# Performance work log

Measured on AMD Instinct MI355X. Metric: run time of the kernel, lower is better.

The kernel has to match this reference:

```python
import jax, jax.numpy as jnp
import numpy as np

B, CIN, COUT, K, H, W = 2, 128, 64, 64, 128, 128
BN_EPS = 1e-5


def setup_inputs() -> dict:
    key = jax.random.key(0)
    k1, k2, k3, k4 = jax.random.split(key, 4)
    x = jax.random.normal(k1, (B, CIN, H, W), dtype=jnp.float32)
    index = jax.random.randint(k2, (B, 1, H, W), 0, K)  # superpixel labels
    # kaiming_uniform(a=sqrt(5)) ~ uniform with bound sqrt(6/((1+5)*fan_in)) = 1/sqrt(fan_in)
    Wft = jax.random.uniform(k3, (CIN, COUT), dtype=jnp.float32,
                             minval=-1.0, maxval=1.0) / np.sqrt(CIN).astype(np.float32)
    Wm = jax.random.uniform(k4, (COUT, COUT), dtype=jnp.float32,
                            minval=-1.0, maxval=1.0) / np.sqrt(COUT).astype(np.float32)
    gamma = jnp.ones((COUT,), jnp.float32)
    beta = jnp.zeros((COUT,), jnp.float32)
    return {"x": x, "index": index, "Wft": Wft, "Wm": Wm, "gamma": gamma, "beta": beta}


def _gnn_forward(x, index, Wft, Wm, gamma, beta):
    # FeatureTransform: [B,Cin,H,W] -> [B,Cout,H,W]
    xt = jnp.einsum('bchw,co->bohw', x, Wft)

    idx = index[:, 0]                                   # [B,H,W]
    oh = jax.nn.one_hot(idx, K, dtype=xt.dtype)         # [B,H,W,K]

    # RegionalMeans (segment-mean over superpixels; equivalent to the
    # repeated-tensor multiply+sum in the torch code, without the 5D blowup)
    block_sum = oh.sum(axis=(1, 2))                     # [B,K]
    sums = jnp.einsum('bhwk,bohw->bko', oh, xt)         # [B,K,Cout]
    denom = block_sum + (block_sum == 0).astype(xt.dtype)
    means = sums / denom[..., None]                     # [B,K,Cout]

    # Adj: pairwise Mahalanobis distance with learned cov = Wm @ Wm.T
    cov = Wm @ Wm.T
    inv_cov = jnp.linalg.inv(cov)
    diff = means[:, :, None, :] - means[:, None, :, :]  # [B,K,K,Cout]
    q = jnp.einsum('bijc,cd,bijd->bij', diff, inv_cov, diff)
    dist = jnp.sqrt(jnp.maximum(q, 1e-12))              # clamp: diagonal q==0
    adj = jnp.exp(-dist)                                # [B,K,K]

    # GCN propagate: adjacency-weighted aggregation of region means
    adj_means = jnp.einsum('bij,bjo->bio', adj, means)  # [B,K,Cout]

    # sum_k one_hot_k * (x_rep + adj_means_k) == xt + gather(adj_means, idx)
    gathered = jnp.take_along_axis(adj_means, idx.reshape(B, -1, 1), axis=1)
    gathered = gathered.reshape(B, H, W, COUT).transpose(0, 3, 1, 2)
    features = jax.nn.relu(xt + gathered)               # [B,Cout,H,W]

    # BatchNorm2d (training-mode batch statistics, biased variance)
    mean = features.mean(axis=(0, 2, 3), keepdims=True)
    var = features.var(axis=(0, 2, 3), keepdims=True)
    out = (features - mean) / jnp.sqrt(var + BN_EPS)
    out = out * gamma[None, :, None, None] + beta[None, :, None, None]
    return out


def reference(x, index, Wft, Wm, gamma, beta):
    return _gnn_forward(x, index, Wft, Wm, gamma, beta)
```

## Files before the change

kernel.cpp:

```cpp
#include <hip/hip_runtime.h>
#include <hip/hip_bf16.h>

#define CIN   128
#define COUT  64
#define HW    16384

typedef __hip_bfloat16 bf16;

#define OFF_XT    0u
#define OFF_PS    1048576u
#define OFF_PC    2097152u
#define OFF_MEANS 2129920u
#define OFF_DIAG  2138112u
#define OFF_INV   2138240u
#define OFF_ADJM  2142336u
#define OFF_BNP   2150528u

__device__ __forceinline__ float rdlane(float v, int lane) {
  return __int_as_float(__builtin_amdgcn_readlane(__float_as_int(v), lane));
}
__device__ __forceinline__ unsigned short f2bfu(float f) {
  union { bf16 h; unsigned short u; } cv; cv.h = __float2bfloat16(f); return cv.u;
}
__device__ __forceinline__ float bf2f(unsigned short u) {
  union { unsigned int i; float f; } cv; cv.i = ((unsigned int)u) << 16; return cv.f;
}

__global__ __launch_bounds__(256, 4) void k1_xt_bins_inv(
    const float* __restrict__ x, const int* __restrict__ index,
    const float* __restrict__ Wft, const float* __restrict__ Wm,
    float* __restrict__ ws)
{
  __shared__ __align__(16) float smem[64 * 68];
  const int blk = blockIdx.x, tid = threadIdx.x;
  if (blk < 1024) {
    float* lds_sums = smem;
    float* lds_cnt  = smem + 2304;
    for (int i = tid; i < 2368; i += 256) smem[i] = 0.f;
    __syncthreads();
    const int b  = blk >> 9;
    const int oh = (blk >> 8) & 1;
    const int ps = blk & 255;
    const int w = tid >> 6, lane = tid & 63;
    const int pq = lane & 7, og = lane >> 3;
    const int px = ps * 64 + (w >> 1) * 32 + pq * 4;
    const int lo = (w & 1) * 16 + og * 2;
    const int o  = oh * 32 + lo;
    const float* xp = x + (size_t)b * CIN * HW + px;
    const float* wp = Wft + o;
    const int4 kv = *(const int4*)(index + b * HW + px);
    float acc[8];
#pragma unroll
    for (int j = 0; j < 8; ++j) acc[j] = 0.f;
#pragma unroll 16
    for (int c = 0; c < 128; ++c) {
      const float4 xv = *(const float4*)xp; xp += HW;
      const float2 wv = *(const float2*)wp; wp += 64;
      acc[0] = fmaf(xv.x, wv.x, acc[0]); acc[1] = fmaf(xv.y, wv.x, acc[1]);
      acc[2] = fmaf(xv.z, wv.x, acc[2]); acc[3] = fmaf(xv.w, wv.x, acc[3]);
      acc[4] = fmaf(xv.x, wv.y, acc[4]); acc[5] = fmaf(xv.y, wv.y, acc[5]);
      acc[6] = fmaf(xv.z, wv.y, acc[6]); acc[7] = fmaf(xv.w, wv.y, acc[7]);
    }
    unsigned short* xtu = (unsigned short*)(ws + OFF_XT);
#pragma unroll
    for (int i = 0; i < 2; ++i) {
      ushort4 u;
      u.x = f2bfu(acc[i*4+0]); u.y = f2bfu(acc[i*4+1]);
      u.z = f2bfu(acc[i*4+2]); u.w = f2bfu(acc[i*4+3]);
      *(ushort4*)(xtu + (size_t)(b * 64 + o + i) * HW + px) = u;
    }
    const int kk[4] = {kv.x, kv.y, kv.z, kv.w};
#pragma unroll
    for (int j = 0; j < 4; ++j) {
      atomicAdd(&lds_sums[kk[j] * 36 + lo    ], acc[j]);
      atomicAdd(&lds_sums[kk[j] * 36 + lo + 1], acc[4 + j]);
    }
    if (oh == 0 && (w & 1) == 0 && og == 0) {
#pragma unroll
      for (int j = 0; j < 4; ++j) atomicAdd(&lds_cnt[kk[j]], 1.f);
    }
    __syncthreads();
    unsigned short* pb = (unsigned short*)(ws + OFF_PS) + (size_t)((b * 2 + oh) * 256 + ps) * 2048;
    {
      const int k = tid >> 2, l0 = (tid & 3) * 8;
      const float4 v0 = *(const float4*)&lds_sums[k * 36 + l0];
      const float4 v1 = *(const float4*)&lds_sums[k * 36 + l0 + 4];
      ushort4 ua, ub;
      ua.x = f2bfu(v0.x); ua.y = f2bfu(v0.y); ua.z = f2bfu(v0.z); ua.w = f2bfu(v0.w);
      ub.x = f2bfu(v1.x); ub.y = f2bfu(v1.y); ub.z = f2bfu(v1.z); ub.w = f2bfu(v1.w);
      unsigned short* pp = pb + k * 32 + l0;
      *(ushort4*)pp = ua; *(ushort4*)(pp + 4) = ub;
    }
    if (oh == 0 && tid < 64)
      ws[OFF_PC + (size_t)(b * 64 + tid) * 256 + ps] = lds_cnt[tid];
  } else {
    float* wm = smem;
    for (int e = tid; e < 4096; e += 256) wm[(e >> 6) * 68 + (e & 63)] = Wm[e];
    __syncthreads();
    const int i0 = (tid >> 4) << 2, j0 = (tid & 15) << 2;
    float c4[16];
#pragma unroll
    for (int q = 0; q < 16; ++q) c4[q] = 0.f;
    for (int cq = 0; cq < 64; cq += 4) {
      float4 a[4], bb[4];
#pragma unroll
      for (int ii = 0; ii < 4; ++ii) a[ii]  = *(const float4*)&wm[(i0+ii)*68 + cq];
#pragma unroll
      for (int jj = 0; jj < 4; ++jj) bb[jj] = *(const float4*)&wm[(j0+jj)*68 + cq];
#pragma unroll
      for (int ii = 0; ii < 4; ++ii)
#pragma unroll
        for (int jj = 0; jj < 4; ++jj)
          c4[ii*4+jj] = fmaf(a[ii].x, bb[jj].x, fmaf(a[ii].y, bb[jj].y,
                        fmaf(a[ii].z, bb[jj].z, fmaf(a[ii].w, bb[jj].w, c4[ii*4+jj]))));
    }
    __syncthreads();
#pragma unroll
    for (int ii = 0; ii < 4; ++ii)
#pragma unroll
      for (int jj = 0; jj < 4; ++jj)
        smem[(i0+ii)*68 + (j0+jj)] = c4[ii*4+jj];
    __syncthreads();
    if (tid < 64) {
      __builtin_amdgcn_s_setprio(3);
      float r[64];
#pragma unroll
      for (int j = 0; j < 64; ++j) r[j] = smem[tid * 68 + j];
#pragma unroll
      for (int k = 0; k < 64; ++k) {
        const float piv = rdlane(r[k], k);
        const float rp  = 1.0f / piv;
        const float a   = (tid == k) ? (rp - 1.0f) : (-r[k] * rp);
#pragma unroll
        for (int j = 0; j < 64; ++j) {
          const float s = rdlane(r[j], k);
          r[j] = fmaf(a, s, r[j]);
        }
        r[k] = (tid == k) ? rp : a;
      }
      __builtin_amdgcn_s_setprio(0);
#pragma unroll
      for (int j = 0; j < 64; ++j) ws[OFF_INV + tid * 64 + j] = r[j];
    }
  }
}

__global__ __launch_bounds__(1024) void k15_means_diag(float* __restrict__ ws)
{
  __shared__ float red[1024];
  __shared__ float lds_c[4];
  __shared__ float lds_m[64];
  const int blk = blockIdx.x, t = threadIdx.x;
  const int b = blk >> 6, k = blk & 63;
  const int o = t & 63, chunk = t >> 6;
  const int oh = o >> 5, o32 = o & 31;
  const unsigned short* psu = (const unsigned short*)(ws + OFF_PS);
  const size_t base = (size_t)((b * 2 + oh) * 256 + chunk * 16) * 2048 + k * 32 + o32;
  float s = 0.f;
#pragma unroll
  for (int i = 0; i < 16; ++i) s += bf2f(psu[base + (size_t)i * 2048]);
  red[chunk * 64 + o] = s;
  float cv = 0.f;
  if (t < 256) cv = ws[OFF_PC + (size_t)(b * 64 + k) * 256 + t];
#pragma unroll
  for (int m = 32; m; m >>= 1) cv += __shfl_xor(cv, m, 64);
  if (t < 256 && (t & 63) == 0) lds_c[t >> 6] = cv;
  __syncthreads();
  if (t < 64) {
    float m_raw = 0.f;
#pragma unroll
    for (int ch = 0; ch < 16; ++ch) m_raw += red[ch * 64 + o];
    const float cnt = lds_c[0] + lds_c[1] + lds_c[2] + lds_c[3];
    const float denom = cnt + ((cnt == 0.f) ? 1.f : 0.f);
    const float m = m_raw / denom;
    ws[OFF_MEANS + (size_t)(b * 64 + k) * 64 + o] = m;
    lds_m[o] = m;
    float inner = 0.f;
#pragma unroll 8
    for (int d = 0; d < 64; ++d) inner = fmaf(ws[OFF_INV + d * 64 + o], lds_m[d], inner);
    float p = m * inner;
#pragma unroll
    for (int mm = 32; mm; mm >>= 1) p += __shfl_xor(p, mm, 64);
    if (o == 0) ws[OFF_DIAG + b * 64 + k] = p;
  }
}

__global__ __launch_bounds__(256) void k2_adj(float* __restrict__ ws)
{
  __shared__ __align__(16) float means_s[64 * 68];
  __shared__ __align__(16) float inv_s[64 * 68];
  __shared__ __align__(16) float T_s[8 * 68];
  __shared__ __align__(16) float adj_s[8 * 68];
  __shared__ float diag_s[64];
  const int b = blockIdx.x >> 3;
  const int i0 = (blockIdx.x & 7) << 3;
  const int t = threadIdx.x;
  const float* mg = ws + OFF_MEANS + b * 4096;
  for (int e = t; e < 4096; e += 256) means_s[(e >> 6) * 68 + (e & 63)] = mg[e];
  const float* ig = ws + OFF_INV;
  for (int e = t; e < 4096; e += 256) inv_s[(e >> 6) * 68 + (e & 63)] = ig[e];
  if (t < 64) diag_s[t] = ws[OFF_DIAG + b * 64 + t];
  __syncthreads();
  if (t < 128) {
    const int i = t >> 4, d0 = (t & 15) << 2;
    float4 acc = {0.f, 0.f, 0.f, 0.f};
    for (int c = 0; c < 64; ++c) {
      const float mv = means_s[(i0 + i) * 68 + c];
      const float4 iv = *(const float4*)&inv_s[c * 68 + d0];
      acc.x = fmaf(mv, iv.x, acc.x); acc.y = fmaf(mv, iv.y, acc.y);
      acc.z = fmaf(mv, iv.z, acc.z); acc.w = fmaf(mv, iv.w, acc.w);
    }
    *(float4*)&T_s[i * 68 + d0] = acc;
  }
  __syncthreads();
  {
    const int i = t >> 5, jb = t & 31;
#pragma unroll
    for (int jj = 0; jj < 2; ++jj) {
      const int j = jb + (jj << 5);
      float4 p4 = {0.f, 0.f, 0.f, 0.f};
      for (int dq = 0; dq < 64; dq += 4) {
        const float4 tv = *(const float4*)&T_s[i * 68 + dq];
        const float4 mv = *(const float4*)&means_s[j * 68 + dq];
        p4.x = fmaf(tv.x, mv.x, p4.x); p4.y = fmaf(tv.y, mv.y, p4.y);
        p4.z = fmaf(tv.z, mv.z, p4.z); p4.w = fmaf(tv.w, mv.w, p4.w);
      }
      const float p = (p4.x + p4.y) + (p4.z + p4.w);
      const float q = diag_s[i0 + i] + diag_s[j] - 2.f * p;
      adj_s[i * 68 + j] = __expf(-sqrtf(fmaxf(q, 1e-12f)));
    }
  }
  __syncthreads();
  if (t < 128) {
    const int i = t >> 4, oq = (t & 15) << 2;
    float4 am = {0.f, 0.f, 0.f, 0.f};
    for (int j = 0; j < 64; ++j) {
      const float av = adj_s[i * 68 + j];
      const float4 mv = *(const float4*)&means_s[j * 68 + oq];
      am.x = fmaf(av, mv.x, am.x); am.y = fmaf(av, mv.y, am.y);
      am.z = fmaf(av, mv.z, am.z); am.w = fmaf(av, mv.w, am.w);
    }
    *(float4*)(ws + OFF_ADJM + (size_t)(b * 64 + i0 + i) * 64 + oq) = am;
  }
}

__global__ __launch_bounds__(256) void k3_bnstats(const int* __restrict__ index,
                                                  float* __restrict__ ws)
{
  __shared__ float am_s[128];
  __shared__ float red[4];
  const int blk = blockIdx.x, t = threadIdx.x;
  const int b = blk >> 8, oc = (blk >> 3) & 31, tile = blk & 7;
  const int o0 = oc * 2;
  if (t < 128) am_s[t] = ws[OFF_ADJM + (size_t)(b * 64 + (t >> 1)) * 64 + o0 + (t & 1)];
  if (t < 4) red[t] = 0.f;
  __syncthreads();
  const int lane = t & 63, w = t >> 6;
  const unsigned short* xtu = (const unsigned short*)(ws + OFF_XT);
  float s0 = 0.f, s1 = 0.f, q0 = 0.f, q1 = 0.f;
#pragma unroll
  for (int q = 0; q < 2; ++q) {
    const int px = tile * 2048 + (w * 2 + q) * 256 + lane * 4;
    const int4 kv = *(const int4*)(index + b * HW + px);
    const ushort4 u0 = *(const ushort4*)(xtu + (size_t)(b * 64 + o0    ) * HW + px);
    const ushort4 u1 = *(const ushort4*)(xtu + (size_t)(b * 64 + o0 + 1) * HW + px);
    const int kk[4] = {kv.x, kv.y, kv.z, kv.w};
    const float x0[4] = {bf2f(u0.x), bf2f(u0.y), bf2f(u0.z), bf2f(u0.w)};
    const float x1[4] = {bf2f(u1.x), bf2f(u1.y), bf2f(u1.z), bf2f(u1.w)};
#pragma unroll
    for (int j = 0; j < 4; ++j) {
      const float2 am = *(const float2*)&am_s[kk[j] * 2];
      const float f0 = fmaxf(x0[j] + am.x, 0.f);
      const float f1 = fmaxf(x1[j] + am.y, 0.f);
      s0 += f0; q0 = fmaf(f0, f0, q0);
      s1 += f1; q1 = fmaf(f1, f1, q1);
    }
  }
#pragma unroll
  for (int m = 1; m < 64; m <<= 1) {
    s0 += __shfl_xor(s0, m, 64); s1 += __shfl_xor(s1, m, 64);
    q0 += __shfl_xor(q0, m, 64); q1 += __shfl_xor(q1, m, 64);
  }
  if (lane == 0) {
    atomicAdd(&red[0], s0); atomicAdd(&red[1], s1);
    atomicAdd(&red[2], q0); atomicAdd(&red[3], q1);
  }
  __syncthreads();
  if (t == 0) {
    float4 v; v.x = red[0]; v.y = red[1]; v.z = red[2]; v.w = red[3];
    *(float4*)(ws + OFF_BNP + (size_t)(oc * 16 + b * 8 + tile) * 4) = v;
  }
}

__global__ __launch_bounds__(256) void k4_out(const int* __restrict__ index,
    const float* __restrict__ gamma, const float* __restrict__ beta,
    const float* __restrict__ ws, float* __restrict__ out)
{
  __shared__ float am_s[128];
  __shared__ float4 tmp[16];
  __shared__ float sc_s[2], sh_s[2];
  const int blk = blockIdx.x, t = threadIdx.x;
  const int b = blk >> 8, oc = (blk >> 3) & 31, tile = blk & 7;
  const int o0 = oc * 2;
  if (t < 128) am_s[t] = ws[OFF_ADJM + (size_t)(b * 64 + (t >> 1)) * 64 + o0 + (t & 1)];
  if (t < 16) tmp[t] = *(const float4*)(ws + OFF_BNP + (size_t)(oc * 16 + t) * 4);
  if (t < 2) {
    float s = 0.f, qq = 0.f;
#pragma unroll
    for (int i = 0; i < 16; ++i) {
      const float4 v = tmp[i];
      s  += (t == 0) ? v.x : v.y;
      qq += (t == 0) ? v.z : v.w;
    }
    const float mean = s * (1.f / 32768.f);
    const float var  = qq * (1.f / 32768.f) - mean * mean;
    const float sc = gamma[o0 + t] * rsqrtf(var + 1e-5f);
    sc_s[t] = sc;
    sh_s[t] = fmaf(-mean, sc, beta[o0 + t]);
  }
  __syncthreads();
  const int lane = t & 63, w = t >> 6;
  const unsigned short* xtu = (const unsigned short*)(ws + OFF_XT);
  const float c0 = sc_s[0], c1 = sc_s[1], h0 = sh_s[0], h1 = sh_s[1];
#pragma unroll
  for (int q = 0; q < 2; ++q) {
    const int px = tile * 2048 + (w * 2 + q) * 256 + lane * 4;
    const int4 kv = *(const int4*)(index + b * HW + px);
    const ushort4 u0 = *(const ushort4*)(xtu + (size_t)(b * 64 + o0    ) * HW + px);
    const ushort4 u1 = *(const ushort4*)(xtu + (size_t)(b * 64 + o0 + 1) * HW + px);
    const int kk[4] = {kv.x, kv.y, kv.z, kv.w};
    const float x0[4] = {bf2f(u0.x), bf2f(u0.y), bf2f(u0.z), bf2f(u0.w)};
    const float x1[4] = {bf2f(u1.x), bf2f(u1.y), bf2f(u1.z), bf2f(u1.w)};
    float4 o4a, o4b;
    float* oa = (float*)&o4a; float* ob = (float*)&o4b;
#pragma unroll
    for (int j = 0; j < 4; ++j) {
      const float2 am = *(const float2*)&am_s[kk[j] * 2];
      oa[j] = fmaf(fmaxf(x0[j] + am.x, 0.f), c0, h0);
      ob[j] = fmaf(fmaxf(x1[j] + am.y, 0.f), c1, h1);
    }
    *(float4*)(out + (size_t)(b * 64 + o0    ) * HW + px) = o4a;
    *(float4*)(out + (size_t)(b * 64 + o0 + 1) * HW + px) = o4b;
  }
}

extern "C" void kernel_launch(void* const* d_in, const int* in_sizes, int n_in,
                              void* d_out, int out_size, void* d_ws, size_t ws_size,
                              hipStream_t stream) {
  const float* x     = (const float*)d_in[0];
  const int*   index = (const int*)d_in[1];
  const float* Wft   = (const float*)d_in[2];
  const float* Wm    = (const float*)d_in[3];
  const float* gamma = (const float*)d_in[4];
  const float* beta  = (const float*)d_in[5];
  float* ws  = (float*)d_ws;
  float* out = (float*)d_out;

  k1_xt_bins_inv<<<1025, 256, 0, stream>>>(x, index, Wft, Wm, ws);
  k15_means_diag<<<128, 1024, 0, stream>>>(ws);
  k2_adj<<<16, 256, 0, stream>>>(ws);
  k3_bnstats<<<512, 256, 0, stream>>>(index, ws);
  k4_out<<<512, 256, 0, stream>>>(index, gamma, beta, ws, out);
}
```

Before: 140.6 us.

## Stage x and Wft tiles in LDS and compute all 64 outputs per block

New measurement: 298.0 us. 2.12x slower.

```diff
diff --git a/kernel.cpp b/kernel.cpp
--- a/kernel.cpp
+++ b/kernel.cpp
@@ -26,73 +26,84 @@
   union { unsigned int i; float f; } cv; cv.i = ((unsigned int)u) << 16; return cv.f;
 }
 
-__global__ __launch_bounds__(256, 4) void k1_xt_bins_inv(
+__global__ __launch_bounds__(256, 2) void k1_xt_bins_inv(
     const float* __restrict__ x, const int* __restrict__ index,
     const float* __restrict__ Wft, const float* __restrict__ Wm,
     float* __restrict__ ws)
 {
-  __shared__ __align__(16) float smem[64 * 68];
+  __shared__ __align__(16) float smem[16384];
   const int blk = blockIdx.x, tid = threadIdx.x;
-  if (blk < 1024) {
-    float* lds_sums = smem;
-    float* lds_cnt  = smem + 2304;
-    for (int i = tid; i < 2368; i += 256) smem[i] = 0.f;
-    __syncthreads();
-    const int b  = blk >> 9;
-    const int oh = (blk >> 8) & 1;
-    const int ps = blk & 255;
-    const int w = tid >> 6, lane = tid & 63;
-    const int pq = lane & 7, og = lane >> 3;
-    const int px = ps * 64 + (w >> 1) * 32 + pq * 4;
-    const int lo = (w & 1) * 16 + og * 2;
-    const int o  = oh * 32 + lo;
-    const float* xp = x + (size_t)b * CIN * HW + px;
-    const float* wp = Wft + o;
+  if (blk < 512) {
+    float* xl = smem;
+    float* wl = smem + 8192;
+    const int b = blk >> 8, ps = blk & 255;
+    const float* xg = x + (size_t)b * CIN * HW + ps * 64;
+#pragma unroll
+    for (int j = 0; j < 8; ++j) {
+      const int fj = j * 256 + tid;
+      const int c = fj >> 4, q4 = (fj & 15) * 4;
+      *(float4*)&xl[c * 64 + q4] = *(const float4*)(xg + (size_t)c * HW + q4);
+      *(float4*)&wl[c * 64 + q4] = *(const float4*)(Wft + c * 64 + q4);
+    }
+    __syncthreads();
+    const int px_grp = tid & 15, o_grp = tid >> 4;
+    const int px = ps * 64 + px_grp * 4, o0 = o_grp * 4;
+    float acc[16];
+#pragma unroll
+    for (int j = 0; j < 16; ++j) acc[j] = 0.f;
+#pragma unroll 8
+    for (int c = 0; c < 128; ++c) {
+      const float4 xv = *(const float4*)&xl[c * 64 + px_grp * 4];
+      const float4 wv = *(const float4*)&wl[c * 64 + o0];
+      acc[ 0]=fmaf(xv.x,wv.x,acc[ 0]); acc[ 1]=fmaf(xv.y,wv.x,acc[ 1]);
+      acc[ 2]=fmaf(xv.z,wv.x,acc[ 2]); acc[ 3]=fmaf(xv.w,wv.x,acc[ 3]);
+      acc[ 4]=fmaf(xv.x,wv.y,acc[ 4]); acc[ 5]=fmaf(xv.y,wv.y,acc[ 5]);
+      acc[ 6]=fmaf(xv.z,wv.y,acc[ 6]); acc[ 7]=fmaf(xv.w,wv.y,acc[ 7]);
+      acc[ 8]=fmaf(xv.x,wv.z,acc[ 8]); acc[ 9]=fmaf(xv.y,wv.z,acc[ 9]);
+      acc[10]=fmaf(xv.z,wv.z,acc[10]); acc[11]=fmaf(xv.w,wv.z,acc[11]);
+      acc[12]=fmaf(xv.x,wv.w,acc[12]); acc[13]=fmaf(xv.y,wv.w,acc[13]);
+      acc[14]=fmaf(xv.z,wv.w,acc[14]); acc[15]=fmaf(xv.w,wv.w,acc[15]);
+    }
+    unsigned short* xtu = (unsigned short*)(ws + OFF_XT);
+#pragma unroll
+    for (int oj = 0; oj < 4; ++oj) {
+      ushort4 u;
+      u.x = f2bfu(acc[oj*4+0]); u.y = f2bfu(acc[oj*4+1]);
+      u.z = f2bfu(acc[oj*4+2]); u.w = f2bfu(acc[oj*4+3]);
+      *(ushort4*)(xtu + (size_t)(b * 64 + o0 + oj) * HW + px) = u;
+    }
     const int4 kv = *(const int4*)(index + b * HW + px);
-    float acc[8];
-#pragma unroll
-    for (int j = 0; j < 8; ++j) acc[j] = 0.f;
-#pragma unroll 16
-    for (int c = 0; c < 128; ++c) {
-      const float4 xv = *(const float4*)xp; xp += HW;
-      const float2 wv = *(const float2*)wp; wp += 64;
-      acc[0] = fmaf(xv.x, wv.x, acc[0]); acc[1] = fmaf(xv.y, wv.x, acc[1]);
-      acc[2] = fmaf(xv.z, wv.x, acc[2]); acc[3] = fmaf(xv.w, wv.x, acc[3]);
-      acc[4] = fmaf(xv.x, wv.y, acc[4]); acc[5] = fmaf(xv.y, wv.y, acc[5]);
-      acc[6] = fmaf(xv.z, wv.y, acc[6]); acc[7] = fmaf(xv.w, wv.y, acc[7]);
-    }
-    unsigned short* xtu = (unsigned short*)(ws + OFF_XT);
-#pragma unroll
-    for (int i = 0; i < 2; ++i) {
-      ushort4 u;
-      u.x = f2bfu(acc[i*4+0]); u.y = f2bfu(acc[i*4+1]);
-      u.z = f2bfu(acc[i*4+2]); u.w = f2bfu(acc[i*4+3]);
-      *(ushort4*)(xtu + (size_t)(b * 64 + o + i) * HW + px) = u;
-    }
     const int kk[4] = {kv.x, kv.y, kv.z, kv.w};
-#pragma unroll
-    for (int j = 0; j < 4; ++j) {
-      atomicAdd(&lds_sums[kk[j] * 36 + lo    ], acc[j]);
-      atomicAdd(&lds_sums[kk[j] * 36 + lo + 1], acc[4 + j]);
-    }
-    if (oh == 0 && (w & 1) == 0 && og == 0) {
-#pragma unroll
-      for (int j = 0; j < 4; ++j) atomicAdd(&lds_cnt[kk[j]], 1.f);
-    }
-    __syncthreads();
-    unsigned short* pb = (unsigned short*)(ws + OFF_PS) + (size_t)((b * 2 + oh) * 256 + ps) * 2048;
+    __syncthreads();
+    float* bins = smem;
+    float* cnt  = smem + 64 * 68;
+    for (int i = tid; i < 64 * 68 + 64; i += 256) smem[i] = 0.f;
+    __syncthreads();
+#pragma unroll
+    for (int pj = 0; pj < 4; ++pj) {
+      const int kb = kk[pj] * 68 + o0;
+      atomicAdd(&bins[kb    ], acc[ 0 + pj]);
+      atomicAdd(&bins[kb + 1], acc[ 4 + pj]);
+      atomicAdd(&bins[kb + 2], acc[ 8 + pj]);
+      atomicAdd(&bins[kb + 3], acc[12 + pj]);
+    }
+    if (o_grp == 0) {
+#pragma unroll
+      for (int pj = 0; pj < 4; ++pj) atomicAdd(&cnt[kk[pj]], 1.f);
+    }
+    __syncthreads();
+    unsigned short* pb = (unsigned short*)(ws + OFF_PS) + (size_t)blk * 4096;
     {
-      const int k = tid >> 2, l0 = (tid & 3) * 8;
-      const float4 v0 = *(const float4*)&lds_sums[k * 36 + l0];
-      const float4 v1 = *(const float4*)&lds_sums[k * 36 + l0 + 4];
-      ushort4 ua, ub;
-      ua.x = f2bfu(v0.x); ua.y = f2bfu(v0.y); ua.z = f2bfu(v0.z); ua.w = f2bfu(v0.w);
-      ub.x = f2bfu(v1.x); ub.y = f2bfu(v1.y); ub.z = f2bfu(v1.z); ub.w = f2bfu(v1.w);
-      unsigned short* pp = pb + k * 32 + l0;
-      *(ushort4*)pp = ua; *(ushort4*)(pp + 4) = ub;
-    }
-    if (oh == 0 && tid < 64)
-      ws[OFF_PC + (size_t)(b * 64 + tid) * 256 + ps] = lds_cnt[tid];
+      const int k = tid >> 2, ob = (tid & 3) * 16;
+#pragma unroll
+      for (int q = 0; q < 4; ++q) {
+        const float4 v = *(const float4*)&bins[k * 68 + ob + q * 4];
+        ushort4 u;
+        u.x = f2bfu(v.x); u.y = f2bfu(v.y); u.z = f2bfu(v.z); u.w = f2bfu(v.w);
+        *(ushort4*)(pb + k * 64 + ob + q * 4) = u;
+      }
+    }
+    if (tid < 64) ws[OFF_PC + (size_t)(b * 64 + tid) * 256 + ps] = cnt[tid];
   } else {
     float* wm = smem;
     for (int e = tid; e < 4096; e += 256) wm[(e >> 6) * 68 + (e & 63)] = Wm[e];
@@ -153,12 +164,13 @@
   const int blk = blockIdx.x, t = threadIdx.x;
   const int b = blk >> 6, k = blk & 63;
   const int o = t & 63, chunk = t >> 6;
-  const int oh = o >> 5, o32 = o & 31;
   const unsigned short* psu = (const unsigned short*)(ws + OFF_PS);
-  const size_t base = (size_t)((b * 2 + oh) * 256 + chunk * 16) * 2048 + k * 32 + o32;
   float s = 0.f;
 #pragma unroll
-  for (int i = 0; i < 16; ++i) s += bf2f(psu[base + (size_t)i * 2048]);
+  for (int i = 0; i < 16; ++i) {
+    const int slab = chunk * 16 + i;
+    s += bf2f(psu[(size_t)(b * 256 + slab) * 4096 + k * 64 + o]);
+  }
   red[chunk * 64 + o] = s;
   float cv = 0.f;
   if (t < 256) cv = ws[OFF_PC + (size_t)(b * 64 + k) * 256 + t];
@@ -356,7 +368,7 @@
   float* ws  = (float*)d_ws;
   float* out = (float*)d_out;
 
-  k1_xt_bins_inv<<<1025, 256, 0, stream>>>(x, index, Wft, Wm, ws);
+  k1_xt_bins_inv<<<513, 256, 0, stream>>>(x, index, Wft, Wm, ws);
   k15_means_diag<<<128, 1024, 0, stream>>>(ws);
   k2_adj<<<16, 256, 0, stream>>>(ws);
   k3_bnstats<<<512, 256, 0, stream>>>(index, ws);
```
